# Optimization experiments

Measured on AMD Instinct MI355X. Metric: run time of the kernel, lower is better.

## Reference

```python
import jax, jax.numpy as jnp
import numpy as np

B, N, D, H = 256, 128, 512, 512

def setup_inputs() -> dict:
    key = jax.random.key(0)
    k1, k2, k3, k4 = jax.random.split(key, 4)
    X = jax.random.normal(k1, (B, N, D), dtype=jnp.float32)
    A = jax.random.uniform(k2, (B, N, N), dtype=jnp.float32)
    # fc: Linear(D, H) params, kaiming-uniform-ish init
    lim = 1.0 / np.sqrt(D)
    W = jax.random.uniform(k3, (H, D), minval=-lim, maxval=lim, dtype=jnp.float32)
    b = jax.random.uniform(k4, (H,), minval=-lim, maxval=lim, dtype=jnp.float32)
    ln_w = jnp.ones((H,), dtype=jnp.float32)
    ln_b = jnp.zeros((H,), dtype=jnp.float32)
    return {"X": X, "A": A, "W": W, "b": b, "ln_w": ln_w, "ln_b": ln_b}

def reference(X, A, W, b, ln_w, ln_b):
    # row-normalize adjacency: A / (sum_j A[b,i,j] + 1e-6)
    A_norm = A / (jnp.sum(A, axis=2, keepdims=True) + 1e-6)
    # aggregate neighbors: (B,N,N) @ (B,N,D) -> (B,N,D)
    X_neighbor = jnp.einsum('bnm,bmd->bnd', A_norm, X)
    X_agg = X + X_neighbor
    # linear D -> H
    X_up = jnp.einsum('bnd,hd->bnh', X_agg, W) + b
    # layernorm over last dim (eps=1e-5 matches torch default)
    mu = jnp.mean(X_up, axis=-1, keepdims=True)
    var = jnp.mean(jnp.square(X_up - mu), axis=-1, keepdims=True)
    X_ln = (X_up - mu) / jnp.sqrt(var + 1e-5) * ln_w + ln_b
    return jax.nn.sigmoid(X_ln)
```

## Files before the change

kernel.cpp:

```cpp
#include <hip/hip_runtime.h>
#include <cstdint>

#define BB 256
#define NN 128
#define DD 512
#define HH 512

typedef __attribute__((ext_vector_type(8))) short bf16x8;
typedef __attribute__((ext_vector_type(16))) float f32x16;
typedef unsigned short u16;

static __device__ __forceinline__ u16 f2bf(float f) {
    union { float f; uint32_t u; } v; v.f = f;
    uint32_t u = v.u;
    return (u16)((u + 0x7FFFu + ((u >> 16) & 1u)) >> 16);
}

static __device__ __forceinline__ void gload16(const u16* g, u16* l) {
    __builtin_amdgcn_global_load_lds((const __attribute__((address_space(1))) void*)g,
                                     (__attribute__((address_space(3))) void*)l, 16, 0, 0);
}

__global__ __launch_bounds__(256) void wconv_kernel(const float* __restrict__ W, u16* __restrict__ Wb) {
    int idx = (blockIdx.x * 256 + threadIdx.x) * 4;
    float4 v = *(const float4*)(W + idx);
    ushort4 o;
    o.x = f2bf(v.x); o.y = f2bf(v.y); o.z = f2bf(v.z); o.w = f2bf(v.w);
    *(ushort4*)(Wb + idx) = o;
}

__global__ __launch_bounds__(512) void agg_kernel(const float* __restrict__ X, const float* __restrict__ A,
                                                  u16* __restrict__ Xagg) {
    __shared__ __align__(16) char smem[163840];
    u16* Ms = (u16*)smem;
    u16* Xt = (u16*)(smem + 32768);

    const int t = threadIdx.x;
    const int lane = t & 63, w = t >> 6, l31 = lane & 31, lh = lane >> 5;
    const int batch = blockIdx.x;
    const int wm = w >> 2, wn = w & 3;

    {
        const int row = t >> 2, seg = t & 3;
        const float* Ag = A + (size_t)batch * NN * NN + row * NN + seg * 32;
        float4 a[8];
        #pragma unroll
        for (int j = 0; j < 8; ++j) a[j] = *(const float4*)(Ag + j * 4);
        float s = 0.f;
        #pragma unroll
        for (int j = 0; j < 8; ++j) s += a[j].x + a[j].y + a[j].z + a[j].w;
        s += __shfl_xor(s, 1);
        s += __shfl_xor(s, 2);
        const float inv = 1.0f / (s + 1e-6f);
        #pragma unroll
        for (int c2 = 0; c2 < 4; ++c2) {
            u16 tmp[8];
            const float* pe = (const float*)&a[c2 * 2];
            #pragma unroll
            for (int e = 0; e < 8; ++e) {
                int m = seg * 32 + c2 * 8 + e;
                tmp[e] = f2bf(pe[e] * inv + (m == row ? 1.0f : 0.0f));
            }
            int c = seg * 4 + c2;
            *(uint4*)(Ms + row * 128 + ((c ^ (row & 15)) << 3)) = *(const uint4*)tmp;
        }
    }

    {
        const float* Xg = X + (size_t)batch * NN * DD;
        #pragma unroll
        for (int it = 0; it < 32; ++it) {
            int q = it * 512 + t;
            int m = q >> 7, c4 = q & 127;
            float4 v = *(const float4*)(Xg + (size_t)m * DD + c4 * 4);
            float fv[4] = {v.x, v.y, v.z, v.w};
            #pragma unroll
            for (int j = 0; j < 4; ++j) {
                int d = c4 * 4 + j;
                Xt[d * 128 + (((m >> 3) ^ ((d >> 2) & 7)) << 3) + (m & 7)] = f2bf(fv[j]);
            }
        }
    }
    __syncthreads();

    u16* Og = Xagg + (size_t)batch * NN * DD;
    #pragma unroll
    for (int dh = 0; dh < 2; ++dh) {
        f32x16 acc1[2][2];
        #pragma unroll
        for (int fi = 0; fi < 2; ++fi)
            #pragma unroll
            for (int fd = 0; fd < 2; ++fd)
                #pragma unroll
                for (int r = 0; r < 16; ++r)
                    acc1[fi][fd][r] = 0.f;

        #pragma unroll
        for (int ksl = 0; ksl < 8; ++ksl) {
            const int kc = ksl * 2 + lh;
            bf16x8 af[2], bx[2];
            #pragma unroll
            for (int fi = 0; fi < 2; ++fi) {
                int i = wm * 64 + fi * 32 + l31;
                af[fi] = *(const bf16x8*)(Ms + i * 128 + ((kc ^ (i & 15)) << 3));
            }
            #pragma unroll
            for (int fd = 0; fd < 2; ++fd) {
                int d = dh * 256 + wn * 64 + fd * 32 + l31;
                bx[fd] = *(const bf16x8*)(Xt + d * 128 + ((kc ^ ((d >> 2) & 7)) << 3));
            }
            #pragma unroll
            for (int fi = 0; fi < 2; ++fi)
                #pragma unroll
                for (int fd = 0; fd < 2; ++fd)
                    acc1[fi][fd] = __builtin_amdgcn_mfma_f32_32x32x16_bf16(af[fi], bx[fd], acc1[fi][fd], 0, 0, 0);
        }

        #pragma unroll
        for (int fi = 0; fi < 2; ++fi)
            #pragma unroll
            for (int r = 0; r < 16; ++r) {
                int i = wm * 64 + fi * 32 + (r & 3) + 8 * (r >> 2) + 4 * lh;
                #pragma unroll
                for (int fd = 0; fd < 2; ++fd) {
                    int d = dh * 256 + wn * 64 + fd * 32 + l31;
                    Og[(size_t)i * DD + d] = f2bf(acc1[fi][fd][r]);
                }
            }
    }
}

__global__ __launch_bounds__(256, 2) void gemm_ln_kernel(const u16* __restrict__ Xagg, const u16* __restrict__ Wb,
                                                         const float* __restrict__ bias, const float* __restrict__ lnw,
                                                         const float* __restrict__ lnb, float* __restrict__ out) {
    __shared__ __align__(16) char smem[65536];
    float* Pss = (float*)smem;
    float* musig = (float*)(smem + 1024);

    const int t = threadIdx.x;
    const int lane = t & 63, w = t >> 6, l31 = lane & 31, lh = lane >> 5;
    const size_t rb = (size_t)blockIdx.x * 32;
    const u16* Xab = Xagg + rb * DD;

    float bias_v[4], lnw_v[4], lnb_v[4];
    #pragma unroll
    for (int fh = 0; fh < 4; ++fh) {
        int h = w * 128 + fh * 32 + l31;
        bias_v[fh] = bias[h];
        lnw_v[fh] = lnw[h];
        lnb_v[fh] = lnb[h];
    }

#define ASTAGE                                                                        \
    {                                                                                 \
        _Pragma("unroll")                                                             \
        for (int it_ = 0; it_ < 8; ++it_) {                                           \
            int q_ = it_ * 256 + t;                                                   \
            int m_ = q_ >> 6, cp_ = q_ & 63;                                          \
            gload16(Xab + (size_t)m_ * DD + ((cp_ ^ (m_ & 15)) * 8),                  \
                    (u16*)smem + q_ * 8);                                             \
        }                                                                             \
    }
#define WSTAGE(KS)                                                                    \
    {                                                                                 \
        u16* wl_ = (u16*)(smem + 32768);                                              \
        _Pragma("unroll")                                                             \
        for (int it_ = 0; it_ < 8; ++it_) {                                           \
            int q_ = it_ * 256 + t;                                                   \
            int h_ = q_ >> 2, cc_ = q_ & 3;                                           \
            gload16(Wb + (size_t)h_ * DD + (KS) * 32 + ((cc_ ^ ((h_ >> 1) & 3)) * 8), \
                    wl_ + q_ * 8);                                                    \
        }                                                                             \
    }

    f32x16 acc[4];
    #pragma unroll
    for (int fh = 0; fh < 4; ++fh)
        #pragma unroll
        for (int r = 0; r < 16; ++r)
            acc[fh][r] = 0.f;

    ASTAGE;
    WSTAGE(0);
    __syncthreads();

    for (int ks = 0; ks < 16; ++ks) {
        const u16* al = (const u16*)smem;
        const u16* wl = (const u16*)(smem + 32768);
        #pragma unroll
        for (int s2 = 0; s2 < 2; ++s2) {
            const int kc = s2 * 2 + lh;
            const int gc = ks * 4 + kc;
            bf16x8 af = *(const bf16x8*)(al + (l31 * 64 + (gc ^ (l31 & 15))) * 8);
            bf16x8 bw[4];
            #pragma unroll
            for (int fh = 0; fh < 4; ++fh) {
                int h = w * 128 + fh * 32 + l31;
                bw[fh] = *(const bf16x8*)(wl + (h * 4 + (kc ^ ((h >> 1) & 3))) * 8);
            }
            #pragma unroll
            for (int fh = 0; fh < 4; ++fh)
                acc[fh] = __builtin_amdgcn_mfma_f32_32x32x16_bf16(af, bw[fh], acc[fh], 0, 0, 0);
        }
        if (ks < 15) {
            __syncthreads();
            WSTAGE(ks + 1);
            __syncthreads();
        }
    }
#undef ASTAGE
#undef WSTAGE
    __syncthreads();

    float rs[16], rss[16];
    #pragma unroll
    for (int r = 0; r < 16; ++r) {
        float s = 0.f, ss = 0.f;
        #pragma unroll
        for (int fh = 0; fh < 4; ++fh) {
            float a = acc[fh][r] + bias_v[fh];
            acc[fh][r] = a;
            s += a; ss += a * a;
        }
        rs[r] = s; rss[r] = ss;
    }
    #pragma unroll
    for (int msk = 1; msk <= 16; msk <<= 1)
        #pragma unroll
        for (int r = 0; r < 16; ++r) {
            rs[r] += __shfl_xor(rs[r], msk);
            rss[r] += __shfl_xor(rss[r], msk);
        }
    if (l31 == 0) {
        #pragma unroll
        for (int r = 0; r < 16; ++r) {
            int rl = (r & 3) + 8 * (r >> 2) + 4 * lh;
            float2 v; v.x = rs[r]; v.y = rss[r];
            *(float2*)(Pss + (w * 32 + rl) * 2) = v;
        }
    }
    __syncthreads();
    if (t < 32) {
        float s = 0.f, ss = 0.f;
        #pragma unroll
        for (int q = 0; q < 4; ++q) {
            float2 v = *(const float2*)(Pss + (q * 32 + t) * 2);
            s += v.x; ss += v.y;
        }
        float mean = s * (1.0f / 512.0f);
        float var = ss * (1.0f / 512.0f) - mean * mean;
        float2 mz; mz.x = mean; mz.y = rsqrtf(var + 1e-5f);
        *(float2*)(musig + t * 2) = mz;
    }
    __syncthreads();

    #pragma unroll
    for (int r = 0; r < 16; ++r) {
        int rl = (r & 3) + 8 * (r >> 2) + 4 * lh;
        float2 mz = *(const float2*)(musig + rl * 2);
        #pragma unroll
        for (int fh = 0; fh < 4; ++fh) {
            float xn = (acc[fh][r] - mz.x) * mz.y * lnw_v[fh] + lnb_v[fh];
            out[(rb + rl) * HH + w * 128 + fh * 32 + l31] = 1.0f / (1.0f + __expf(-xn));
        }
    }
}

extern "C" void kernel_launch(void* const* d_in, const int* in_sizes, int n_in,
                              void* d_out, int out_size, void* d_ws, size_t ws_size,
                              hipStream_t stream) {
    const float* X = (const float*)d_in[0];
    const float* A = (const float*)d_in[1];
    const float* W = (const float*)d_in[2];
    const float* bias = (const float*)d_in[3];
    const float* lnw = (const float*)d_in[4];
    const float* lnb = (const float*)d_in[5];
    float* out = (float*)d_out;

    u16* Xagg = (u16*)d_ws;
    u16* Wb = (u16*)d_ws + (size_t)BB * NN * DD;

    hipLaunchKernelGGL(wconv_kernel, dim3(256), dim3(256), 0, stream, W, Wb);
    hipLaunchKernelGGL(agg_kernel, dim3(256), dim3(512), 0, stream, X, A, Xagg);
    hipLaunchKernelGGL(gemm_ln_kernel, dim3(1024), dim3(256), 0, stream, Xagg, Wb, bias, lnw, lnb, out);
}
```

Baseline: 88.16 us.

## Read bf16 weights directly from global in k-chunk-major layout, drop W LDS staging

The weight conversion kernel now writes W in a k-chunk-major layout (d/8, h, 8), so each lane's 16-byte fragment is a coalesced global load. The GEMM+LayerNorm kernel drops the per-k-step LDS staging of W and its two barriers per step, keeping only the X tile in LDS. Halving shared memory allows launch bounds of 4 blocks per CU for more occupancy. In exchange, W fragments come from L2/global with latency that is no longer hidden by a double-buffered stage, and register pressure under the stricter launch bound may rise.

```diff
diff --git a/kernel.cpp b/kernel.cpp
--- a/kernel.cpp
+++ b/kernel.cpp
@@ -21,12 +21,13 @@
                                      (__attribute__((address_space(3))) void*)l, 16, 0, 0);
 }
 
-__global__ __launch_bounds__(256) void wconv_kernel(const float* __restrict__ W, u16* __restrict__ Wb) {
+__global__ __launch_bounds__(256) void wconv_kernel(const float* __restrict__ W, u16* __restrict__ Wt) {
     int idx = (blockIdx.x * 256 + threadIdx.x) * 4;
+    int h = idx >> 9, d = idx & 511;
     float4 v = *(const float4*)(W + idx);
     ushort4 o;
     o.x = f2bf(v.x); o.y = f2bf(v.y); o.z = f2bf(v.z); o.w = f2bf(v.w);
-    *(ushort4*)(Wb + idx) = o;
+    *(ushort4*)(Wt + ((size_t)(d >> 3) * HH + h) * 8 + (d & 7)) = o;
 }
 
 __global__ __launch_bounds__(512) void agg_kernel(const float* __restrict__ X, const float* __restrict__ A,
@@ -130,10 +131,10 @@
     }
 }
 
-__global__ __launch_bounds__(256, 2) void gemm_ln_kernel(const u16* __restrict__ Xagg, const u16* __restrict__ Wb,
+__global__ __launch_bounds__(256, 4) void gemm_ln_kernel(const u16* __restrict__ Xagg, const u16* __restrict__ Wt,
                                                          const float* __restrict__ bias, const float* __restrict__ lnw,
                                                          const float* __restrict__ lnb, float* __restrict__ out) {
-    __shared__ __align__(16) char smem[65536];
+    __shared__ __align__(16) char smem[32768];
     float* Pss = (float*)smem;
     float* musig = (float*)(smem + 1024);
 
@@ -151,27 +152,13 @@
         lnb_v[fh] = lnb[h];
     }
 
-#define ASTAGE                                                                        \
-    {                                                                                 \
-        _Pragma("unroll")                                                             \
-        for (int it_ = 0; it_ < 8; ++it_) {                                           \
-            int q_ = it_ * 256 + t;                                                   \
-            int m_ = q_ >> 6, cp_ = q_ & 63;                                          \
-            gload16(Xab + (size_t)m_ * DD + ((cp_ ^ (m_ & 15)) * 8),                  \
-                    (u16*)smem + q_ * 8);                                             \
-        }                                                                             \
-    }
-#define WSTAGE(KS)                                                                    \
-    {                                                                                 \
-        u16* wl_ = (u16*)(smem + 32768);                                              \
-        _Pragma("unroll")                                                             \
-        for (int it_ = 0; it_ < 8; ++it_) {                                           \
-            int q_ = it_ * 256 + t;                                                   \
-            int h_ = q_ >> 2, cc_ = q_ & 3;                                           \
-            gload16(Wb + (size_t)h_ * DD + (KS) * 32 + ((cc_ ^ ((h_ >> 1) & 3)) * 8), \
-                    wl_ + q_ * 8);                                                    \
-        }                                                                             \
-    }
+    #pragma unroll
+    for (int it = 0; it < 8; ++it) {
+        int q = it * 256 + t;
+        int m = q >> 6, cp = q & 63;
+        gload16(Xab + (size_t)m * DD + ((cp ^ (m & 15)) * 8), (u16*)smem + q * 8);
+    }
+    __syncthreads();
 
     f32x16 acc[4];
     #pragma unroll
@@ -180,36 +167,21 @@
         for (int r = 0; r < 16; ++r)
             acc[fh][r] = 0.f;
 
-    ASTAGE;
-    WSTAGE(0);
-    __syncthreads();
-
-    for (int ks = 0; ks < 16; ++ks) {
-        const u16* al = (const u16*)smem;
-        const u16* wl = (const u16*)(smem + 32768);
-        #pragma unroll
-        for (int s2 = 0; s2 < 2; ++s2) {
-            const int kc = s2 * 2 + lh;
-            const int gc = ks * 4 + kc;
-            bf16x8 af = *(const bf16x8*)(al + (l31 * 64 + (gc ^ (l31 & 15))) * 8);
-            bf16x8 bw[4];
-            #pragma unroll
-            for (int fh = 0; fh < 4; ++fh) {
-                int h = w * 128 + fh * 32 + l31;
-                bw[fh] = *(const bf16x8*)(wl + (h * 4 + (kc ^ ((h >> 1) & 3))) * 8);
-            }
-            #pragma unroll
-            for (int fh = 0; fh < 4; ++fh)
-                acc[fh] = __builtin_amdgcn_mfma_f32_32x32x16_bf16(af, bw[fh], acc[fh], 0, 0, 0);
-        }
-        if (ks < 15) {
-            __syncthreads();
-            WSTAGE(ks + 1);
-            __syncthreads();
-        }
-    }
-#undef ASTAGE
-#undef WSTAGE
+    const u16* al = (const u16*)smem;
+    #pragma unroll
+    for (int st = 0; st < 32; ++st) {
+        const int gc = st * 2 + lh;
+        bf16x8 af = *(const bf16x8*)(al + (l31 * 64 + (gc ^ (l31 & 15))) * 8);
+        bf16x8 bw[4];
+        #pragma unroll
+        for (int fh = 0; fh < 4; ++fh) {
+            int h = w * 128 + fh * 32 + l31;
+            bw[fh] = *(const bf16x8*)(Wt + ((size_t)gc * HH + h) * 8);
+        }
+        #pragma unroll
+        for (int fh = 0; fh < 4; ++fh)
+            acc[fh] = __builtin_amdgcn_mfma_f32_32x32x16_bf16(af, bw[fh], acc[fh], 0, 0, 0);
+    }
     __syncthreads();
 
     float rs[16], rss[16];
@@ -278,9 +250,9 @@
     float* out = (float*)d_out;
 
     u16* Xagg = (u16*)d_ws;
-    u16* Wb = (u16*)d_ws + (size_t)BB * NN * DD;
-
-    hipLaunchKernelGGL(wconv_kernel, dim3(256), dim3(256), 0, stream, W, Wb);
+    u16* Wt = (u16*)d_ws + (size_t)BB * NN * DD;
+
+    hipLaunchKernelGGL(wconv_kernel, dim3(256), dim3(256), 0, stream, W, Wt);
     hipLaunchKernelGGL(agg_kernel, dim3(256), dim3(512), 0, stream, X, A, Xagg);
-    hipLaunchKernelGGL(gemm_ln_kernel, dim3(1024), dim3(256), 0, stream, Xagg, Wb, bias, lnw, lnb, out);
-}
+    hipLaunchKernelGGL(gemm_ln_kernel, dim3(1024), dim3(256), 0, stream, Xagg, Wt, bias, lnw, lnb, out);
+}
```

Result: slower. 95.33 us (+8.1%).
